# Kernel tuning notes

Hardware: AMD Instinct MI355X
Metric: run time of the kernel (lower is better)

Reference implementation:

```python
import jax, jax.numpy as jnp
import numpy as np

N = 100000
E = 3200000
D_IN = 128
H = 32   # 2 * out_channels
OUT = 16 # out_channels


def _glorot(key, shape):
    lim = np.sqrt(6.0 / (shape[0] + shape[1]))
    return jax.random.uniform(key, shape, jnp.float32, -lim, lim)


def setup_inputs() -> dict:
    key = jax.random.key(0)
    ks = jax.random.split(key, 8)
    x = jax.random.normal(ks[0], (N, D_IN), jnp.float32)
    edge_index = jax.random.randint(ks[1], (2, E), 0, N, jnp.int64)
    W1 = _glorot(ks[2], (D_IN, H));  b1 = jnp.zeros((H,), jnp.float32)
    Wm = _glorot(ks[3], (H, OUT));   bm = jnp.zeros((OUT,), jnp.float32)
    Wv = _glorot(ks[4], (H, 1));     bv = jnp.zeros((1,), jnp.float32)
    return {"x": x, "edge_index": edge_index,
            "W1": W1, "b1": b1, "Wm": Wm, "bm": bm, "Wv": Wv, "bv": bv}


def _gcn_norm(edge_index, n_nodes):
    # add self-loops, then symmetric normalization D^-1/2 (A+I) D^-1/2
    loop = jnp.arange(n_nodes, dtype=edge_index.dtype)
    src = jnp.concatenate([edge_index[0], loop])
    dst = jnp.concatenate([edge_index[1], loop])
    deg = jax.ops.segment_sum(jnp.ones_like(dst, jnp.float32), dst,
                              num_segments=n_nodes)
    dinv = jnp.where(deg > 0, jax.lax.rsqrt(deg), 0.0)
    norm = dinv[src] * dinv[dst]  # [E + N]
    return src, dst, norm


def _gcn_conv(h, W, b, src, dst, norm, n_nodes):
    h = h @ W                                   # [N, out]
    msg = norm[:, None] * h[src]                # gather + scale, [E+N, out]
    out = jax.ops.segment_sum(msg, dst, num_segments=n_nodes)  # scatter-add
    return out + b


def reference(x, edge_index, W1, b1, Wm, bm, Wv, bv):
    src, dst, norm = _gcn_norm(edge_index, N)
    h = jax.nn.relu(_gcn_conv(x, W1, b1, src, dst, norm, N))
    mean = _gcn_conv(h, Wm, bm, src, dst, norm, N)
    mean = mean / jnp.linalg.norm(mean, axis=-1, keepdims=True)
    var = _gcn_conv(h, Wv, bv, src, dst, norm, N)
    var = jax.nn.softplus(var) + 1.0
    return mean, var
```

## Files before the change

kernel.cpp:

```cpp
#include <hip/hip_runtime.h>
#include <math.h>

#define N_NODES   100000
#define N_EDGES   3200000
#define D_IN      128
#define H_DIM     32
#define OUT_DIM   16
#define NB        391
#define B1        256
#define CHUNK     12500

typedef _Float16 half_t;
typedef __attribute__((ext_vector_type(4))) _Float16 half4;


__global__ __launch_bounds__(256) void k_p1_hist(const int* __restrict__ dst,
                                                 int* __restrict__ hist_g) {
    __shared__ int hist[NB];
    int t = threadIdx.x;
    for (int i = t; i < NB; i += 256) hist[i] = 0;
    __syncthreads();
    int base = blockIdx.x * CHUNK;
    for (int k = t; k < CHUNK; k += 256) {
        int e = base + k;
        if (e < N_EDGES) atomicAdd(&hist[dst[e] >> 8], 1);
    }
    __syncthreads();
    for (int i = t; i < NB; i += 256) hist_g[i * B1 + blockIdx.x] = hist[i];
}


__global__ __launch_bounds__(256) void k_scanA(const int* __restrict__ hist_g,
                                               int* __restrict__ sums) {
    __shared__ int s[256];
    int t = threadIdx.x;
    s[t] = hist_g[blockIdx.x * 256 + t];
    __syncthreads();
    for (int off = 128; off > 0; off >>= 1) {
        if (t < off) s[t] += s[t + off];
        __syncthreads();
    }
    if (t == 0) sums[blockIdx.x] = s[0];
}

__global__ __launch_bounds__(512) void k_scanB(int* sums) {
    __shared__ int a[512], b[512];
    int t = threadIdx.x;
    a[t] = (t < NB) ? sums[t] : 0;
    __syncthreads();
    int* cur = a; int* nxt = b;
    for (int off = 1; off < 512; off <<= 1) {
        nxt[t] = cur[t] + ((t >= off) ? cur[t - off] : 0);
        __syncthreads();
        int* tmp = cur; cur = nxt; nxt = tmp;
    }
    if (t < NB) sums[t] = (t == 0) ? 0 : cur[t - 1];
}

__global__ __launch_bounds__(256) void k_scanC(int* hist_g, const int* __restrict__ sums) {
    __shared__ int a[256], b[256];
    int t = threadIdx.x;
    int v = hist_g[blockIdx.x * 256 + t];
    a[t] = v;
    __syncthreads();
    int* cur = a; int* nxt = b;
    for (int off = 1; off < 256; off <<= 1) {
        nxt[t] = cur[t] + ((t >= off) ? cur[t - off] : 0);
        __syncthreads();
        int* tmp = cur; cur = nxt; nxt = tmp;
    }
    hist_g[blockIdx.x * 256 + t] = sums[blockIdx.x] + cur[t] - v;
}


__global__ __launch_bounds__(256) void k_p3(const int* __restrict__ src,
                                            const int* __restrict__ dst,
                                            const int* __restrict__ hist_g,
                                            unsigned int* __restrict__ pairs) {
    __shared__ int cur[NB];
    int t = threadIdx.x;
    for (int i = t; i < NB; i += 256) cur[i] = hist_g[i * B1 + blockIdx.x];
    __syncthreads();
    int base = blockIdx.x * CHUNK;
    for (int k = t; k < CHUNK; k += 256) {
        int e = base + k;
        if (e < N_EDGES) {
            int d = dst[e];
            int pos = atomicAdd(&cur[d >> 8], 1);
            pairs[pos] = ((unsigned int)(d & 255) << 17) | (unsigned int)src[e];
        }
    }
}


__global__ __launch_bounds__(256) void k_p4(const unsigned int* __restrict__ pairs,
                                            const int* __restrict__ hist_g,
                                            int* __restrict__ csr_src,
                                            int* __restrict__ row_ptr,
                                            float* __restrict__ dinv) {
    __shared__ int cnt[256], a[256], b[256], cur[256];
    int t = threadIdx.x;
    int bk = blockIdx.x;
    int lo = hist_g[bk * 256];
    int hi = (bk + 1 < NB) ? hist_g[(bk + 1) * 256] : N_EDGES;

    cnt[t] = 0;
    __syncthreads();
    for (int j = lo + t; j < hi; j += 256)
        atomicAdd(&cnt[pairs[j] >> 17], 1);
    __syncthreads();

    a[t] = cnt[t];
    __syncthreads();
    int* c0 = a; int* c1 = b;
    for (int off = 1; off < 256; off <<= 1) {
        c1[t] = c0[t] + ((t >= off) ? c0[t - off] : 0);
        __syncthreads();
        int* tmp = c0; c0 = c1; c1 = tmp;
    }
    int excl = c0[t] - cnt[t];
    cur[t] = lo + excl;

    int node = bk * 256 + t;
    if (node < N_NODES) {
        row_ptr[node] = lo + excl;
        dinv[node] = rsqrtf((float)cnt[t] + 1.0f);
    }
    if (bk == NB - 1 && t == 0) row_ptr[N_NODES] = N_EDGES;
    __syncthreads();

    for (int j = lo + t; j < hi; j += 256) {
        unsigned int p = pairs[j];
        int pos = atomicAdd(&cur[p >> 17], 1);
        csr_src[pos] = (int)(p & 0x1FFFFu);
    }
}


__global__ __launch_bounds__(256) void k_gemm1(const float* __restrict__ x,
                                               const float* __restrict__ W1,
                                               const float* __restrict__ dinv,
                                               half_t* __restrict__ hs) {
    int i = blockIdx.x * 256 + threadIdx.x;
    if (i >= N_NODES) return;

    const float* xr = x + (size_t)i * D_IN;
    float acc[H_DIM];
#pragma unroll
    for (int c = 0; c < H_DIM; ++c) acc[c] = 0.f;

    for (int k0 = 0; k0 < D_IN; k0 += 4) {
        float4 xv = *(const float4*)(xr + k0);
#pragma unroll
        for (int kk = 0; kk < 4; ++kk) {
            float xk = (kk == 0) ? xv.x : (kk == 1) ? xv.y : (kk == 2) ? xv.z : xv.w;
            const float* wr = W1 + (k0 + kk) * H_DIM;
#pragma unroll
            for (int c = 0; c < H_DIM; ++c)
                acc[c] = fmaf(xk, wr[c], acc[c]);
        }
    }

    float di = dinv[i];
    half_t* o = hs + (size_t)i * H_DIM;
#pragma unroll
    for (int c4 = 0; c4 < H_DIM / 4; ++c4) {
        half4 ov;
        ov.x = (half_t)(acc[c4 * 4 + 0] * di);
        ov.y = (half_t)(acc[c4 * 4 + 1] * di);
        ov.z = (half_t)(acc[c4 * 4 + 2] * di);
        ov.w = (half_t)(acc[c4 * 4 + 3] * di);
        *(half4*)(o + c4 * 4) = ov;
    }
}


__global__ __launch_bounds__(256) void k_gather1(const int* __restrict__ row_ptr,
                                                 const int* __restrict__ csr_src,
                                                 const float* __restrict__ dinv,
                                                 const half_t* __restrict__ hs,
                                                 const float* __restrict__ b1,
                                                 half_t* __restrict__ h) {
    int t = blockIdx.x * 256 + threadIdx.x;
    int i = t >> 3, c = t & 7;

    int start = row_ptr[i], end = row_ptr[i + 1];
    half4 sv = *(const half4*)(hs + (size_t)i * H_DIM + c * 4);
    float4 acc;
    acc.x = (float)sv.x; acc.y = (float)sv.y; acc.z = (float)sv.z; acc.w = (float)sv.w;

    int j = start;
    for (; j + 8 <= end; j += 8) {
        int s0 = csr_src[j + 0], s1 = csr_src[j + 1], s2 = csr_src[j + 2], s3 = csr_src[j + 3];
        int s4 = csr_src[j + 4], s5 = csr_src[j + 5], s6 = csr_src[j + 6], s7 = csr_src[j + 7];
        half4 v0 = *(const half4*)(hs + (size_t)s0 * H_DIM + c * 4);
        half4 v1 = *(const half4*)(hs + (size_t)s1 * H_DIM + c * 4);
        half4 v2 = *(const half4*)(hs + (size_t)s2 * H_DIM + c * 4);
        half4 v3 = *(const half4*)(hs + (size_t)s3 * H_DIM + c * 4);
        half4 v4 = *(const half4*)(hs + (size_t)s4 * H_DIM + c * 4);
        half4 v5 = *(const half4*)(hs + (size_t)s5 * H_DIM + c * 4);
        half4 v6 = *(const half4*)(hs + (size_t)s6 * H_DIM + c * 4);
        half4 v7 = *(const half4*)(hs + (size_t)s7 * H_DIM + c * 4);
        acc.x += (float)v0.x + (float)v1.x + (float)v2.x + (float)v3.x
               + (float)v4.x + (float)v5.x + (float)v6.x + (float)v7.x;
        acc.y += (float)v0.y + (float)v1.y + (float)v2.y + (float)v3.y
               + (float)v4.y + (float)v5.y + (float)v6.y + (float)v7.y;
        acc.z += (float)v0.z + (float)v1.z + (float)v2.z + (float)v3.z
               + (float)v4.z + (float)v5.z + (float)v6.z + (float)v7.z;
        acc.w += (float)v0.w + (float)v1.w + (float)v2.w + (float)v3.w
               + (float)v4.w + (float)v5.w + (float)v6.w + (float)v7.w;
    }
    for (; j < end; ++j) {
        int s = csr_src[j];
        half4 v = *(const half4*)(hs + (size_t)s * H_DIM + c * 4);
        acc.x += (float)v.x; acc.y += (float)v.y; acc.z += (float)v.z; acc.w += (float)v.w;
    }

    float di = dinv[i];
    float4 bb = *(const float4*)(b1 + c * 4);
    half4 o;
    o.x = (half_t)fmaxf(di * acc.x + bb.x, 0.f);
    o.y = (half_t)fmaxf(di * acc.y + bb.y, 0.f);
    o.z = (half_t)fmaxf(di * acc.z + bb.z, 0.f);
    o.w = (half_t)fmaxf(di * acc.w + bb.w, 0.f);
    *(half4*)(h + (size_t)i * H_DIM + c * 4) = o;
}


__global__ __launch_bounds__(256) void k_gemm2(const half_t* __restrict__ h,
                                               const float* __restrict__ Wm,
                                               const float* __restrict__ Wv,
                                               const float* __restrict__ dinv,
                                               half_t* __restrict__ hmv,
                                               float* __restrict__ varr) {
    int i = blockIdx.x * 256 + threadIdx.x;
    if (i >= N_NODES) return;

    const half4* hp = (const half4*)(h + (size_t)i * H_DIM);
    float acc[OUT_DIM + 1];
#pragma unroll
    for (int c = 0; c <= OUT_DIM; ++c) acc[c] = 0.f;

#pragma unroll
    for (int k4 = 0; k4 < H_DIM / 4; ++k4) {
        half4 v = hp[k4];
#pragma unroll
        for (int kk = 0; kk < 4; ++kk) {
            int k = k4 * 4 + kk;
            float hv = (kk == 0) ? (float)v.x : (kk == 1) ? (float)v.y
                     : (kk == 2) ? (float)v.z : (float)v.w;
            const float* wr = Wm + k * OUT_DIM;
#pragma unroll
            for (int c = 0; c < OUT_DIM; ++c)
                acc[c] = fmaf(hv, wr[c], acc[c]);
            acc[OUT_DIM] = fmaf(hv, Wv[k], acc[OUT_DIM]);
        }
    }

    float di = dinv[i];
    half_t* o = hmv + (size_t)i * OUT_DIM;
#pragma unroll
    for (int c4 = 0; c4 < OUT_DIM / 4; ++c4) {
        half4 ov;
        ov.x = (half_t)(acc[c4 * 4 + 0] * di);
        ov.y = (half_t)(acc[c4 * 4 + 1] * di);
        ov.z = (half_t)(acc[c4 * 4 + 2] * di);
        ov.w = (half_t)(acc[c4 * 4 + 3] * di);
        *(half4*)(o + c4 * 4) = ov;
    }
    varr[i] = acc[OUT_DIM] * di;
}


__global__ __launch_bounds__(256) void k_gather2f(const int* __restrict__ row_ptr,
                                                  const int* __restrict__ csr_src,
                                                  const float* __restrict__ dinv,
                                                  const half_t* __restrict__ hmv,
                                                  const float* __restrict__ varr,
                                                  const float* __restrict__ bm,
                                                  const float* __restrict__ bv,
                                                  float* __restrict__ out) {
    int t = blockIdx.x * 256 + threadIdx.x;
    int i = t >> 3, c = t & 7;

    int start = row_ptr[i], end = row_ptr[i + 1];
    float4 acc = make_float4(0.f, 0.f, 0.f, 0.f);
    float va = 0.f;
    if (c < 4) {
        half4 sv = *(const half4*)(hmv + (size_t)i * OUT_DIM + c * 4);
        acc.x = (float)sv.x; acc.y = (float)sv.y; acc.z = (float)sv.z; acc.w = (float)sv.w;
    } else if (c == 4) {
        va = varr[i];
    }

    int j = start;
    for (; j + 8 <= end; j += 8) {
        int s0 = csr_src[j + 0], s1 = csr_src[j + 1], s2 = csr_src[j + 2], s3 = csr_src[j + 3];
        int s4 = csr_src[j + 4], s5 = csr_src[j + 5], s6 = csr_src[j + 6], s7 = csr_src[j + 7];
        if (c < 4) {
            half4 v0 = *(const half4*)(hmv + (size_t)s0 * OUT_DIM + c * 4);
            half4 v1 = *(const half4*)(hmv + (size_t)s1 * OUT_DIM + c * 4);
            half4 v2 = *(const half4*)(hmv + (size_t)s2 * OUT_DIM + c * 4);
            half4 v3 = *(const half4*)(hmv + (size_t)s3 * OUT_DIM + c * 4);
            half4 v4 = *(const half4*)(hmv + (size_t)s4 * OUT_DIM + c * 4);
            half4 v5 = *(const half4*)(hmv + (size_t)s5 * OUT_DIM + c * 4);
            half4 v6 = *(const half4*)(hmv + (size_t)s6 * OUT_DIM + c * 4);
            half4 v7 = *(const half4*)(hmv + (size_t)s7 * OUT_DIM + c * 4);
            acc.x += (float)v0.x + (float)v1.x + (float)v2.x + (float)v3.x
                   + (float)v4.x + (float)v5.x + (float)v6.x + (float)v7.x;
            acc.y += (float)v0.y + (float)v1.y + (float)v2.y + (float)v3.y
                   + (float)v4.y + (float)v5.y + (float)v6.y + (float)v7.y;
            acc.z += (float)v0.z + (float)v1.z + (float)v2.z + (float)v3.z
                   + (float)v4.z + (float)v5.z + (float)v6.z + (float)v7.z;
            acc.w += (float)v0.w + (float)v1.w + (float)v2.w + (float)v3.w
                   + (float)v4.w + (float)v5.w + (float)v6.w + (float)v7.w;
        } else if (c == 4) {
            va += varr[s0] + varr[s1] + varr[s2] + varr[s3]
                + varr[s4] + varr[s5] + varr[s6] + varr[s7];
        }
    }
    for (; j < end; ++j) {
        int s = csr_src[j];
        if (c < 4) {
            half4 v = *(const half4*)(hmv + (size_t)s * OUT_DIM + c * 4);
            acc.x += (float)v.x; acc.y += (float)v.y; acc.z += (float)v.z; acc.w += (float)v.w;
        } else if (c == 4) {
            va += varr[s];
        }
    }

    float di = dinv[i];
    float4 r;
    float ssp = 0.f;
    if (c < 4) {
        float4 bb = *(const float4*)(bm + c * 4);
        r.x = di * acc.x + bb.x;
        r.y = di * acc.y + bb.y;
        r.z = di * acc.z + bb.z;
        r.w = di * acc.w + bb.w;
        ssp = r.x * r.x + r.y * r.y + r.z * r.z + r.w * r.w;
    }
    ssp += __shfl_xor(ssp, 1, 8);
    ssp += __shfl_xor(ssp, 2, 8);
    ssp += __shfl_xor(ssp, 4, 8);
    float inv = rsqrtf(ssp);

    if (c < 4) {
        float4 o;
        o.x = r.x * inv; o.y = r.y * inv; o.z = r.z * inv; o.w = r.w * inv;
        *(float4*)(out + (size_t)i * OUT_DIM + c * 4) = o;
    } else if (c == 4) {
        float xv = di * va + bv[0];
        float sp = fmaxf(xv, 0.f) + log1pf(expf(-fabsf(xv)));
        out[(size_t)N_NODES * OUT_DIM + i] = sp + 1.0f;
    }
}


extern "C" void kernel_launch(void* const* d_in, const int* in_sizes, int n_in,
                              void* d_out, int out_size, void* d_ws, size_t ws_size,
                              hipStream_t stream) {
    const float* x  = (const float*)d_in[0];
    const int*   ei = (const int*)d_in[1];
    const float* W1 = (const float*)d_in[2];
    const float* b1 = (const float*)d_in[3];
    const float* Wm = (const float*)d_in[4];
    const float* bm = (const float*)d_in[5];
    const float* Wv = (const float*)d_in[6];
    const float* bv = (const float*)d_in[7];
    float* out = (float*)d_out;

    const int* src = ei;
    const int* dst = ei + N_EDGES;

    int*   wsi     = (int*)d_ws;
    int*   csr_src = wsi;
    int*   row_ptr = csr_src + N_EDGES;
    float* dinv    = (float*)(row_ptr + N_NODES + 1);
    int*   hist_g  = (int*)(dinv + N_NODES);
    int*   sums    = hist_g + NB * B1;
    size_t off     = (size_t)(sums + 512 - wsi);
    off = (off + 3) & ~(size_t)3;
    unsigned int* pairs = (unsigned int*)(wsi + off);
    half_t* hs     = (half_t*)pairs;
    half_t* h      = hs + (size_t)N_NODES * H_DIM;
    half_t* hmv    = h + (size_t)N_NODES * H_DIM;
    float*  varr   = (float*)(hmv + (size_t)N_NODES * OUT_DIM);

    const int B = 256;
    int gN  = (N_NODES + B - 1) / B;
    int gN8 = (N_NODES * 8 + B - 1) / B;

    k_p1_hist<<<B1, B, 0, stream>>>(dst, hist_g);
    k_scanA<<<NB, B, 0, stream>>>(hist_g, sums);
    k_scanB<<<1, 512, 0, stream>>>(sums);
    k_scanC<<<NB, B, 0, stream>>>(hist_g, sums);
    k_p3<<<B1, B, 0, stream>>>(src, dst, hist_g, pairs);
    k_p4<<<NB, B, 0, stream>>>(pairs, hist_g, csr_src, row_ptr, dinv);

    k_gemm1<<<gN, B, 0, stream>>>(x, W1, dinv, hs);
    k_gather1<<<gN8, B, 0, stream>>>(row_ptr, csr_src, dinv, hs, b1, h);

    k_gemm2<<<gN, B, 0, stream>>>(h, Wm, Wv, dinv, hmv, varr);
    k_gather2f<<<gN8, B, 0, stream>>>(row_ptr, csr_src, dinv, hmv, varr, bm, bv, out);
}
```

Baseline: 318.2 us.

## Double sort blocks, widen gather vectors, and pack gather2 into 4 lanes

The edge-sort pass now splits the edges into twice as many chunks (512 instead of 256), so the multi-level scan is resized and scanB now has each thread scan four sums. k_p4 runs with 512 threads per bucket. gather1 uses 4 lanes per node, each loading 8 halves, which halves the thread count and index loads. gather2 drops the idle lanes by using 4 lanes per node and splits the variance gather across those lanes, at the cost of extra shuffles and a smaller unroll.

```diff
diff --git a/kernel.cpp b/kernel.cpp
--- a/kernel.cpp
+++ b/kernel.cpp
@@ -7,11 +7,14 @@
 #define H_DIM     32
 #define OUT_DIM   16
 #define NB        391
-#define B1        256
-#define CHUNK     12500
+#define B1        512
+#define CHUNK     6250
+#define NHIST     (NB * B1)
+#define SUMS_N    (NHIST / 256)
 
 typedef _Float16 half_t;
 typedef __attribute__((ext_vector_type(4))) _Float16 half4;
+typedef __attribute__((ext_vector_type(8))) _Float16 half8;
 
 
 __global__ __launch_bounds__(256) void k_p1_hist(const int* __restrict__ dst,
@@ -21,10 +24,8 @@
     for (int i = t; i < NB; i += 256) hist[i] = 0;
     __syncthreads();
     int base = blockIdx.x * CHUNK;
-    for (int k = t; k < CHUNK; k += 256) {
-        int e = base + k;
-        if (e < N_EDGES) atomicAdd(&hist[dst[e] >> 8], 1);
-    }
+    for (int k = t; k < CHUNK; k += 256)
+        atomicAdd(&hist[dst[base + k] >> 8], 1);
     __syncthreads();
     for (int i = t; i < NB; i += 256) hist_g[i * B1 + blockIdx.x] = hist[i];
 }
@@ -43,25 +44,16 @@
     if (t == 0) sums[blockIdx.x] = s[0];
 }
 
-__global__ __launch_bounds__(512) void k_scanB(int* sums) {
-    __shared__ int a[512], b[512];
-    int t = threadIdx.x;
-    a[t] = (t < NB) ? sums[t] : 0;
-    __syncthreads();
-    int* cur = a; int* nxt = b;
-    for (int off = 1; off < 512; off <<= 1) {
-        nxt[t] = cur[t] + ((t >= off) ? cur[t - off] : 0);
-        __syncthreads();
-        int* tmp = cur; cur = nxt; nxt = tmp;
-    }
-    if (t < NB) sums[t] = (t == 0) ? 0 : cur[t - 1];
-}
-
-__global__ __launch_bounds__(256) void k_scanC(int* hist_g, const int* __restrict__ sums) {
+__global__ __launch_bounds__(256) void k_scanB(int* sums) {
     __shared__ int a[256], b[256];
     int t = threadIdx.x;
-    int v = hist_g[blockIdx.x * 256 + t];
-    a[t] = v;
+    int base = t * 4;
+    int v0 = (base + 0 < SUMS_N) ? sums[base + 0] : 0;
+    int v1 = (base + 1 < SUMS_N) ? sums[base + 1] : 0;
+    int v2 = (base + 2 < SUMS_N) ? sums[base + 2] : 0;
+    int v3 = (base + 3 < SUMS_N) ? sums[base + 3] : 0;
+    int i1 = v0 + v1, i2 = i1 + v2, i3 = i2 + v3;
+    a[t] = i3;
     __syncthreads();
     int* cur = a; int* nxt = b;
     for (int off = 1; off < 256; off <<= 1) {
@@ -69,6 +61,25 @@
         __syncthreads();
         int* tmp = cur; cur = nxt; nxt = tmp;
     }
+    int excl = cur[t] - i3;
+    if (base + 0 < SUMS_N) sums[base + 0] = excl;
+    if (base + 1 < SUMS_N) sums[base + 1] = excl + v0;
+    if (base + 2 < SUMS_N) sums[base + 2] = excl + i1;
+    if (base + 3 < SUMS_N) sums[base + 3] = excl + i2;
+}
+
+__global__ __launch_bounds__(256) void k_scanC(int* hist_g, const int* __restrict__ sums) {
+    __shared__ int a[256], b[256];
+    int t = threadIdx.x;
+    int v = hist_g[blockIdx.x * 256 + t];
+    a[t] = v;
+    __syncthreads();
+    int* cur = a; int* nxt = b;
+    for (int off = 1; off < 256; off <<= 1) {
+        nxt[t] = cur[t] + ((t >= off) ? cur[t - off] : 0);
+        __syncthreads();
+        int* tmp = cur; cur = nxt; nxt = tmp;
+    }
     hist_g[blockIdx.x * 256 + t] = sums[blockIdx.x] + cur[t] - v;
 }
 
@@ -84,16 +95,14 @@
     int base = blockIdx.x * CHUNK;
     for (int k = t; k < CHUNK; k += 256) {
         int e = base + k;
-        if (e < N_EDGES) {
-            int d = dst[e];
-            int pos = atomicAdd(&cur[d >> 8], 1);
-            pairs[pos] = ((unsigned int)(d & 255) << 17) | (unsigned int)src[e];
-        }
-    }
-}
-
-
-__global__ __launch_bounds__(256) void k_p4(const unsigned int* __restrict__ pairs,
+        int d = dst[e];
+        int pos = atomicAdd(&cur[d >> 8], 1);
+        pairs[pos] = ((unsigned int)(d & 255) << 17) | (unsigned int)src[e];
+    }
+}
+
+
+__global__ __launch_bounds__(512) void k_p4(const unsigned int* __restrict__ pairs,
                                             const int* __restrict__ hist_g,
                                             int* __restrict__ csr_src,
                                             int* __restrict__ row_ptr,
@@ -101,35 +110,36 @@
     __shared__ int cnt[256], a[256], b[256], cur[256];
     int t = threadIdx.x;
     int bk = blockIdx.x;
-    int lo = hist_g[bk * 256];
-    int hi = (bk + 1 < NB) ? hist_g[(bk + 1) * 256] : N_EDGES;
-
-    cnt[t] = 0;
-    __syncthreads();
-    for (int j = lo + t; j < hi; j += 256)
+    int lo = hist_g[bk * B1];
+    int hi = (bk + 1 < NB) ? hist_g[(bk + 1) * B1] : N_EDGES;
+
+    if (t < 256) cnt[t] = 0;
+    __syncthreads();
+    for (int j = lo + t; j < hi; j += 512)
         atomicAdd(&cnt[pairs[j] >> 17], 1);
     __syncthreads();
 
-    a[t] = cnt[t];
+    if (t < 256) a[t] = cnt[t];
     __syncthreads();
     int* c0 = a; int* c1 = b;
     for (int off = 1; off < 256; off <<= 1) {
-        c1[t] = c0[t] + ((t >= off) ? c0[t - off] : 0);
+        if (t < 256) c1[t] = c0[t] + ((t >= off) ? c0[t - off] : 0);
         __syncthreads();
         int* tmp = c0; c0 = c1; c1 = tmp;
     }
-    int excl = c0[t] - cnt[t];
-    cur[t] = lo + excl;
-
-    int node = bk * 256 + t;
-    if (node < N_NODES) {
-        row_ptr[node] = lo + excl;
-        dinv[node] = rsqrtf((float)cnt[t] + 1.0f);
-    }
-    if (bk == NB - 1 && t == 0) row_ptr[N_NODES] = N_EDGES;
-    __syncthreads();
-
-    for (int j = lo + t; j < hi; j += 256) {
+    if (t < 256) {
+        int excl = c0[t] - cnt[t];
+        cur[t] = lo + excl;
+        int node = bk * 256 + t;
+        if (node < N_NODES) {
+            row_ptr[node] = lo + excl;
+            dinv[node] = rsqrtf((float)cnt[t] + 1.0f);
+        }
+        if (bk == NB - 1 && t == 0) row_ptr[N_NODES] = N_EDGES;
+    }
+    __syncthreads();
+
+    for (int j = lo + t; j < hi; j += 512) {
         unsigned int p = pairs[j];
         int pos = atomicAdd(&cur[p >> 17], 1);
         csr_src[pos] = (int)(p & 0x1FFFFu);
@@ -182,48 +192,53 @@
                                                  const float* __restrict__ b1,
                                                  half_t* __restrict__ h) {
     int t = blockIdx.x * 256 + threadIdx.x;
-    int i = t >> 3, c = t & 7;
-
+    int i = t >> 2, c = t & 3;
+    if (i >= N_NODES) return;
+
+    const half8* hp = (const half8*)hs;
     int start = row_ptr[i], end = row_ptr[i + 1];
-    half4 sv = *(const half4*)(hs + (size_t)i * H_DIM + c * 4);
-    float4 acc;
-    acc.x = (float)sv.x; acc.y = (float)sv.y; acc.z = (float)sv.z; acc.w = (float)sv.w;
+    half8 sv = hp[(size_t)i * 4 + c];
+    float acc[8];
+#pragma unroll
+    for (int k = 0; k < 8; ++k) acc[k] = (float)sv[k];
 
     int j = start;
     for (; j + 8 <= end; j += 8) {
         int s0 = csr_src[j + 0], s1 = csr_src[j + 1], s2 = csr_src[j + 2], s3 = csr_src[j + 3];
         int s4 = csr_src[j + 4], s5 = csr_src[j + 5], s6 = csr_src[j + 6], s7 = csr_src[j + 7];
-        half4 v0 = *(const half4*)(hs + (size_t)s0 * H_DIM + c * 4);
-        half4 v1 = *(const half4*)(hs + (size_t)s1 * H_DIM + c * 4);
-        half4 v2 = *(const half4*)(hs + (size_t)s2 * H_DIM + c * 4);
-        half4 v3 = *(const half4*)(hs + (size_t)s3 * H_DIM + c * 4);
-        half4 v4 = *(const half4*)(hs + (size_t)s4 * H_DIM + c * 4);
-        half4 v5 = *(const half4*)(hs + (size_t)s5 * H_DIM + c * 4);
-        half4 v6 = *(const half4*)(hs + (size_t)s6 * H_DIM + c * 4);
-        half4 v7 = *(const half4*)(hs + (size_t)s7 * H_DIM + c * 4);
-        acc.x += (float)v0.x + (float)v1.x + (float)v2.x + (float)v3.x
-               + (float)v4.x + (float)v5.x + (float)v6.x + (float)v7.x;
-        acc.y += (float)v0.y + (float)v1.y + (float)v2.y + (float)v3.y
-               + (float)v4.y + (float)v5.y + (float)v6.y + (float)v7.y;
-        acc.z += (float)v0.z + (float)v1.z + (float)v2.z + (float)v3.z
-               + (float)v4.z + (float)v5.z + (float)v6.z + (float)v7.z;
-        acc.w += (float)v0.w + (float)v1.w + (float)v2.w + (float)v3.w
-               + (float)v4.w + (float)v5.w + (float)v6.w + (float)v7.w;
+        half8 v0 = hp[(size_t)s0 * 4 + c];
+        half8 v1 = hp[(size_t)s1 * 4 + c];
+        half8 v2 = hp[(size_t)s2 * 4 + c];
+        half8 v3 = hp[(size_t)s3 * 4 + c];
+        half8 v4 = hp[(size_t)s4 * 4 + c];
+        half8 v5 = hp[(size_t)s5 * 4 + c];
+        half8 v6 = hp[(size_t)s6 * 4 + c];
+        half8 v7 = hp[(size_t)s7 * 4 + c];
+#pragma unroll
+        for (int k = 0; k < 8; ++k)
+            acc[k] += ((float)v0[k] + (float)v1[k] + (float)v2[k] + (float)v3[k])
+                    + ((float)v4[k] + (float)v5[k] + (float)v6[k] + (float)v7[k]);
     }
     for (; j < end; ++j) {
         int s = csr_src[j];
-        half4 v = *(const half4*)(hs + (size_t)s * H_DIM + c * 4);
-        acc.x += (float)v.x; acc.y += (float)v.y; acc.z += (float)v.z; acc.w += (float)v.w;
+        half8 v = hp[(size_t)s * 4 + c];
+#pragma unroll
+        for (int k = 0; k < 8; ++k) acc[k] += (float)v[k];
     }
 
     float di = dinv[i];
-    float4 bb = *(const float4*)(b1 + c * 4);
-    half4 o;
-    o.x = (half_t)fmaxf(di * acc.x + bb.x, 0.f);
-    o.y = (half_t)fmaxf(di * acc.y + bb.y, 0.f);
-    o.z = (half_t)fmaxf(di * acc.z + bb.z, 0.f);
-    o.w = (half_t)fmaxf(di * acc.w + bb.w, 0.f);
-    *(half4*)(h + (size_t)i * H_DIM + c * 4) = o;
+    float4 ba = *(const float4*)(b1 + c * 8);
+    float4 bb = *(const float4*)(b1 + c * 8 + 4);
+    half8 o;
+    o[0] = (half_t)fmaxf(di * acc[0] + ba.x, 0.f);
+    o[1] = (half_t)fmaxf(di * acc[1] + ba.y, 0.f);
+    o[2] = (half_t)fmaxf(di * acc[2] + ba.z, 0.f);
+    o[3] = (half_t)fmaxf(di * acc[3] + ba.w, 0.f);
+    o[4] = (half_t)fmaxf(di * acc[4] + bb.x, 0.f);
+    o[5] = (half_t)fmaxf(di * acc[5] + bb.y, 0.f);
+    o[6] = (half_t)fmaxf(di * acc[6] + bb.z, 0.f);
+    o[7] = (half_t)fmaxf(di * acc[7] + bb.w, 0.f);
+    ((half8*)h)[(size_t)i * 4 + c] = o;
 }
 
 
@@ -281,75 +296,52 @@
                                                   const float* __restrict__ bv,
                                                   float* __restrict__ out) {
     int t = blockIdx.x * 256 + threadIdx.x;
-    int i = t >> 3, c = t & 7;
+    int i = t >> 2, c = t & 3;
+    if (i >= N_NODES) return;
 
     int start = row_ptr[i], end = row_ptr[i + 1];
-    float4 acc = make_float4(0.f, 0.f, 0.f, 0.f);
-    float va = 0.f;
-    if (c < 4) {
-        half4 sv = *(const half4*)(hmv + (size_t)i * OUT_DIM + c * 4);
-        acc.x = (float)sv.x; acc.y = (float)sv.y; acc.z = (float)sv.z; acc.w = (float)sv.w;
-    } else if (c == 4) {
-        va = varr[i];
-    }
+    half4 sv = *(const half4*)(hmv + (size_t)i * OUT_DIM + c * 4);
+    float a0 = (float)sv.x, a1 = (float)sv.y, a2 = (float)sv.z, a3 = (float)sv.w;
+    float va = (c == 0) ? varr[i] : 0.f;
 
     int j = start;
-    for (; j + 8 <= end; j += 8) {
+    for (; j + 4 <= end; j += 4) {
         int s0 = csr_src[j + 0], s1 = csr_src[j + 1], s2 = csr_src[j + 2], s3 = csr_src[j + 3];
-        int s4 = csr_src[j + 4], s5 = csr_src[j + 5], s6 = csr_src[j + 6], s7 = csr_src[j + 7];
-        if (c < 4) {
-            half4 v0 = *(const half4*)(hmv + (size_t)s0 * OUT_DIM + c * 4);
-            half4 v1 = *(const half4*)(hmv + (size_t)s1 * OUT_DIM + c * 4);
-            half4 v2 = *(const half4*)(hmv + (size_t)s2 * OUT_DIM + c * 4);
-            half4 v3 = *(const half4*)(hmv + (size_t)s3 * OUT_DIM + c * 4);
-            half4 v4 = *(const half4*)(hmv + (size_t)s4 * OUT_DIM + c * 4);
-            half4 v5 = *(const half4*)(hmv + (size_t)s5 * OUT_DIM + c * 4);
-            half4 v6 = *(const half4*)(hmv + (size_t)s6 * OUT_DIM + c * 4);
-            half4 v7 = *(const half4*)(hmv + (size_t)s7 * OUT_DIM + c * 4);
-            acc.x += (float)v0.x + (float)v1.x + (float)v2.x + (float)v3.x
-                   + (float)v4.x + (float)v5.x + (float)v6.x + (float)v7.x;
-            acc.y += (float)v0.y + (float)v1.y + (float)v2.y + (float)v3.y
-                   + (float)v4.y + (float)v5.y + (float)v6.y + (float)v7.y;
-            acc.z += (float)v0.z + (float)v1.z + (float)v2.z + (float)v3.z
-                   + (float)v4.z + (float)v5.z + (float)v6.z + (float)v7.z;
-            acc.w += (float)v0.w + (float)v1.w + (float)v2.w + (float)v3.w
-                   + (float)v4.w + (float)v5.w + (float)v6.w + (float)v7.w;
-        } else if (c == 4) {
-            va += varr[s0] + varr[s1] + varr[s2] + varr[s3]
-                + varr[s4] + varr[s5] + varr[s6] + varr[s7];
-        }
+        half4 v0 = *(const half4*)(hmv + (size_t)s0 * OUT_DIM + c * 4);
+        half4 v1 = *(const half4*)(hmv + (size_t)s1 * OUT_DIM + c * 4);
+        half4 v2 = *(const half4*)(hmv + (size_t)s2 * OUT_DIM + c * 4);
+        half4 v3 = *(const half4*)(hmv + (size_t)s3 * OUT_DIM + c * 4);
+        a0 += (float)v0.x + (float)v1.x + (float)v2.x + (float)v3.x;
+        a1 += (float)v0.y + (float)v1.y + (float)v2.y + (float)v3.y;
+        a2 += (float)v0.z + (float)v1.z + (float)v2.z + (float)v3.z;
+        a3 += (float)v0.w + (float)v1.w + (float)v2.w + (float)v3.w;
+        int sc = (c == 0) ? s0 : (c == 1) ? s1 : (c == 2) ? s2 : s3;
+        va += varr[sc];
     }
     for (; j < end; ++j) {
         int s = csr_src[j];
-        if (c < 4) {
-            half4 v = *(const half4*)(hmv + (size_t)s * OUT_DIM + c * 4);
-            acc.x += (float)v.x; acc.y += (float)v.y; acc.z += (float)v.z; acc.w += (float)v.w;
-        } else if (c == 4) {
-            va += varr[s];
-        }
+        half4 v = *(const half4*)(hmv + (size_t)s * OUT_DIM + c * 4);
+        a0 += (float)v.x; a1 += (float)v.y; a2 += (float)v.z; a3 += (float)v.w;
+        if (c == 0) va += varr[s];
     }
 
     float di = dinv[i];
-    float4 r;
-    float ssp = 0.f;
-    if (c < 4) {
-        float4 bb = *(const float4*)(bm + c * 4);
-        r.x = di * acc.x + bb.x;
-        r.y = di * acc.y + bb.y;
-        r.z = di * acc.z + bb.z;
-        r.w = di * acc.w + bb.w;
-        ssp = r.x * r.x + r.y * r.y + r.z * r.z + r.w * r.w;
-    }
-    ssp += __shfl_xor(ssp, 1, 8);
-    ssp += __shfl_xor(ssp, 2, 8);
-    ssp += __shfl_xor(ssp, 4, 8);
+    float4 bb = *(const float4*)(bm + c * 4);
+    float r0 = di * a0 + bb.x;
+    float r1 = di * a1 + bb.y;
+    float r2 = di * a2 + bb.z;
+    float r3 = di * a3 + bb.w;
+    float ssp = r0 * r0 + r1 * r1 + r2 * r2 + r3 * r3;
+    ssp += __shfl_xor(ssp, 1, 4);
+    ssp += __shfl_xor(ssp, 2, 4);
+    va  += __shfl_xor(va, 1, 4);
+    va  += __shfl_xor(va, 2, 4);
     float inv = rsqrtf(ssp);
 
-    if (c < 4) {
-        float4 o;
-        o.x = r.x * inv; o.y = r.y * inv; o.z = r.z * inv; o.w = r.w * inv;
-        *(float4*)(out + (size_t)i * OUT_DIM + c * 4) = o;
-    } else if (c == 4) {
+    float4 o;
+    o.x = r0 * inv; o.y = r1 * inv; o.z = r2 * inv; o.w = r3 * inv;
+    *(float4*)(out + (size_t)i * OUT_DIM + c * 4) = o;
+    if (c == 0) {
         float xv = di * va + bv[0];
         float sp = fmaxf(xv, 0.f) + log1pf(expf(-fabsf(xv)));
         out[(size_t)N_NODES * OUT_DIM + i] = sp + 1.0f;
@@ -378,8 +370,8 @@
     int*   row_ptr = csr_src + N_EDGES;
     float* dinv    = (float*)(row_ptr + N_NODES + 1);
     int*   hist_g  = (int*)(dinv + N_NODES);
-    int*   sums    = hist_g + NB * B1;
-    size_t off     = (size_t)(sums + 512 - wsi);
+    int*   sums    = hist_g + NHIST;
+    size_t off     = (size_t)(sums + 1024 - wsi);
     off = (off + 3) & ~(size_t)3;
     unsigned int* pairs = (unsigned int*)(wsi + off);
     half_t* hs     = (half_t*)pairs;
@@ -389,18 +381,18 @@
 
     const int B = 256;
     int gN  = (N_NODES + B - 1) / B;
-    int gN8 = (N_NODES * 8 + B - 1) / B;
+    int gN4 = (N_NODES * 4 + B - 1) / B;
 
     k_p1_hist<<<B1, B, 0, stream>>>(dst, hist_g);
-    k_scanA<<<NB, B, 0, stream>>>(hist_g, sums);
-    k_scanB<<<1, 512, 0, stream>>>(sums);
-    k_scanC<<<NB, B, 0, stream>>>(hist_g, sums);
+    k_scanA<<<SUMS_N, B, 0, stream>>>(hist_g, sums);
+    k_scanB<<<1, B, 0, stream>>>(sums);
+    k_scanC<<<SUMS_N, B, 0, stream>>>(hist_g, sums);
     k_p3<<<B1, B, 0, stream>>>(src, dst, hist_g, pairs);
-    k_p4<<<NB, B, 0, stream>>>(pairs, hist_g, csr_src, row_ptr, dinv);
+    k_p4<<<NB, 512, 0, stream>>>(pairs, hist_g, csr_src, row_ptr, dinv);
 
     k_gemm1<<<gN, B, 0, stream>>>(x, W1, dinv, hs);
-    k_gather1<<<gN8, B, 0, stream>>>(row_ptr, csr_src, dinv, hs, b1, h);
+    k_gather1<<<gN4, B, 0, stream>>>(row_ptr, csr_src, dinv, hs, b1, h);
 
     k_gemm2<<<gN, B, 0, stream>>>(h, Wm, Wv, dinv, hmv, varr);
-    k_gather2f<<<gN8, B, 0, stream>>>(row_ptr, csr_src, dinv, hmv, varr, bm, bv, out);
-}
+    k_gather2f<<<gN4, B, 0, stream>>>(row_ptr, csr_src, dinv, hmv, varr, bm, bv, out);
+}
```

Measured after the change: 315.0 us. Within noise of the previous version (-1.0%).
